# Performance work log

Hardware: AMD Instinct MI355X
Metric: run time of the kernel (lower is better)

Reference implementation:

```python
import jax, jax.numpy as jnp
import numpy as np

D = 1024
LD = 64
NTR = 8192
NT = 8192
DY = 128

def setup_inputs() -> dict:
    key = jax.random.key(0)
    k1, k2, k3, k4 = jax.random.split(key, 4)
    xtr = jax.random.normal(k1, (NTR, D), dtype=jnp.float32)
    ytr = jax.random.normal(k2, (NTR, DY), dtype=jnp.float32)
    xt = jax.random.normal(k3, (NT, D), dtype=jnp.float32)
    A = jax.random.normal(k4, (D, LD), dtype=jnp.float32) / (D ** 0.5)
    return {"xtr": xtr, "ytr": ytr, "xt": xt, "A": A}

def reference(xtr, ytr, xt, A):
    # mean-center both train and test features with the train mean
    mu = jnp.mean(xtr, axis=0, keepdims=True)          # [1, d]
    qtr = (xtr - mu) @ A                                # [Ntr, ld]
    qt = (xt - mu) @ A                                  # [Nt, ld]
    scores = jnp.einsum('nl,ml->nm', qt, qtr)           # [Nt, Ntr]
    E = jax.nn.softmax(scores, axis=1)                  # row-wise softmax over train points
    return E @ ytr                                      # [Nt, dy]
```

## Files before the change

kernel.cpp:

```cpp
#include <hip/hip_runtime.h>
#include <hip/hip_bf16.h>

#define D    1024
#define LD   64
#define NTR  8192
#define NT   8192
#define DY   128

#define SHIFT 40.0f
#define NCHUNK 8
#define CHUNK (NTR / NCHUNK)

typedef __attribute__((ext_vector_type(8))) short bf16x8;
typedef __attribute__((ext_vector_type(4))) short short4_;
typedef __attribute__((ext_vector_type(4))) float f4;

static __device__ __forceinline__ short f2bf(float f) {
    __hip_bfloat16 h = __float2bfloat16(f);
    short s; __builtin_memcpy(&s, &h, 2); return s;
}
static __device__ __forceinline__ float bf2f(short s) {
    __hip_bfloat16 h; __builtin_memcpy(&h, &s, 2); return __bfloat162float(h);
}

static __device__ __forceinline__ void gload_lds16(const void* g, void* l) {
    __builtin_amdgcn_global_load_lds(
        (const __attribute__((address_space(1))) unsigned int*)g,
        (__attribute__((address_space(3))) unsigned int*)l,
        16, 0, 0);
}

__global__ __launch_bounds__(256) void proj_prep(const float* __restrict__ xt,
                                                 const float* __restrict__ xtr,
                                                 const float* __restrict__ A,
                                                 const float* __restrict__ ytr,
                                                 short* __restrict__ qt_hi,
                                                 short* __restrict__ qt_lo,
                                                 short* __restrict__ ktr_hi,
                                                 short* __restrict__ ktr_lo,
                                                 float* __restrict__ muAp,
                                                 short* __restrict__ vtile) {
    __shared__ __align__(16) float smem[4224];

    int tid = threadIdx.x;
    int b = blockIdx.x;

    if (b >= 1024) {
        float* tile = smem;
        int bz = b - 1024;
        int t0 = (bz & 127) * 64;
        int d0 = (bz >> 7) * 64;
        int c = tid & 63;
        int r4 = tid >> 6;
        #pragma unroll
        for (int i = 0; i < 16; ++i) {
            int r = i * 4 + r4;
            tile[r * 66 + c] = ytr[(long)(t0 + r) * DY + d0 + c];
        }
        __syncthreads();
        #pragma unroll
        for (int i = 0; i < 16; ++i) {
            int r = i * 4 + r4;
            int t = t0 + c;
            int dy = d0 + r;
            long idx = (long)(t >> 5) * 4096 + (long)dy * 32
                     + ((((t >> 3) & 3) ^ (dy & 3)) << 3) + (t & 7);
            vtile[idx] = f2bf(tile[c * 66 + r]);
        }
        return;
    }

    float (*xbuf)[2][1024] = (float (*)[2][1024])smem;

    int wave = tid >> 6;
    int lane = tid & 63;
    int quad = lane >> 4;
    int l16 = lane & 15;

    bool is_test = b < (NT / 16);
    int row0 = (is_test ? b : b - NT / 16) * 16;
    const float* x = is_test ? xt : xtr;

    int lr = wave * 4 + (lane >> 4);
    int cg = (lane & 15) ^ (lr & 7);
    const float* xsrc = x + (long)(row0 + lr) * D + cg * 4;

    int col = wave * 16 + l16;
    const float* Acol = A + col;

    f4 acc = (f4){0.f, 0.f, 0.f, 0.f};

    int pr0 = ((quad * 2) ^ (l16 & 7)) * 4;
    int pr1 = (((quad * 2) | 1) ^ (l16 & 7)) * 4;

    gload_lds16(xsrc, &xbuf[0][0][wave * 256]);
    gload_lds16(xsrc + 64, &xbuf[0][1][wave * 256]);
    __syncthreads();

    #pragma unroll 1
    for (int s = 0; s < 8; ++s) {
        int cur = s & 1;
        if (s < 7) {
            const float* nsrc = xsrc + (s + 1) * 128;
            gload_lds16(nsrc, &xbuf[cur ^ 1][0][wave * 256]);
            gload_lds16(nsrc + 64, &xbuf[cur ^ 1][1][wave * 256]);
        }

        #pragma unroll
        for (int s2 = 0; s2 < 2; ++s2) {
            int k0 = s * 128 + s2 * 64;

            bf16x8 bh0, bh1, bl0, bl1;
            #pragma unroll
            for (int j = 0; j < 8; ++j) {
                float a0 = Acol[(long)(k0 + quad * 8 + j) * LD];
                float a1 = Acol[(long)(k0 + 32 + quad * 8 + j) * LD];
                short h0 = f2bf(a0);
                short h1 = f2bf(a1);
                bh0[j] = h0; bl0[j] = f2bf(a0 - bf2f(h0));
                bh1[j] = h1; bl1[j] = f2bf(a1 - bf2f(h1));
            }

            const float* xrow = &xbuf[cur][s2][l16 * 64];
            bf16x8 ah[2], al[2];
            #pragma unroll
            for (int h = 0; h < 2; ++h) {
                f4 v0 = *(const f4*)(xrow + h * 32 + pr0);
                f4 v1 = *(const f4*)(xrow + h * 32 + pr1);
                #pragma unroll
                for (int e = 0; e < 4; ++e) {
                    short hi0 = f2bf(v0[e]);
                    short hi1 = f2bf(v1[e]);
                    ah[h][e]     = hi0;
                    ah[h][e + 4] = hi1;
                    al[h][e]     = f2bf(v0[e] - bf2f(hi0));
                    al[h][e + 4] = f2bf(v1[e] - bf2f(hi1));
                }
            }
            acc = __builtin_amdgcn_mfma_f32_16x16x32_bf16(ah[0], bh0, acc, 0, 0, 0);
            acc = __builtin_amdgcn_mfma_f32_16x16x32_bf16(al[0], bh0, acc, 0, 0, 0);
            acc = __builtin_amdgcn_mfma_f32_16x16x32_bf16(ah[0], bl0, acc, 0, 0, 0);
            acc = __builtin_amdgcn_mfma_f32_16x16x32_bf16(ah[1], bh1, acc, 0, 0, 0);
            acc = __builtin_amdgcn_mfma_f32_16x16x32_bf16(al[1], bh1, acc, 0, 0, 0);
            acc = __builtin_amdgcn_mfma_f32_16x16x32_bf16(ah[1], bl1, acc, 0, 0, 0);
        }
        __syncthreads();
    }

    #pragma unroll
    for (int r = 0; r < 4; ++r) {
        int grow = row0 + quad * 4 + r;
        float qv = acc[r];
        short hi = f2bf(qv);
        short lo = f2bf(qv - bf2f(hi));
        if (is_test) {
            qt_hi[(long)grow * LD + col] = hi;
            qt_lo[(long)grow * LD + col] = lo;
        } else {
            int tl = grow & 31;
            long idx = (long)(grow >> 5) * 2048 + tl * 64
                     + ((((col >> 3) ^ (tl & 7))) << 3) + (col & 7);
            ktr_hi[idx] = hi;
            ktr_lo[idx] = lo;
        }
    }

    if (!is_test) {
        float s = acc[0] + acc[1] + acc[2] + acc[3];
        s += __shfl_xor(s, 16);
        s += __shfl_xor(s, 32);
        if (quad == 0) muAp[(long)(b - NT / 16) * 64 + col] = s;
    }
}

__global__ __launch_bounds__(256) void c_kernel(const short* __restrict__ ktr_hi,
                                                const short* __restrict__ ktr_lo,
                                                const float* __restrict__ muAp,
                                                float* __restrict__ cc) {
    __shared__ float red[4][64];
    __shared__ __align__(16) float muAs[64];
    int l = threadIdx.x & 63;
    int g = threadIdx.x >> 6;
    float ms = 0.f;
    #pragma unroll 8
    for (int p = g; p < 512; p += 4) ms += muAp[(long)p * 64 + l];
    red[g][l] = ms;
    __syncthreads();
    if (threadIdx.x < 64)
        muAs[l] = (red[0][l] + red[1][l] + red[2][l] + red[3][l]) *
                  (1.0f / (float)NTR);
    __syncthreads();

    int t = blockIdx.x * 256 + threadIdx.x;
    int tl = t & 31;
    long rb = (long)(t >> 5) * 2048 + tl * 64;
    float s = SHIFT;
    #pragma unroll
    for (int c = 0; c < 8; ++c) {
        int pos = (c ^ (tl & 7)) << 3;
        bf16x8 h8 = *(const bf16x8*)&ktr_hi[rb + pos];
        bf16x8 l8 = *(const bf16x8*)&ktr_lo[rb + pos];
        f4 m0 = *(const f4*)&muAs[c * 8];
        f4 m1 = *(const f4*)&muAs[c * 8 + 4];
        #pragma unroll
        for (int j = 0; j < 4; ++j) {
            s += (bf2f(h8[j]) + bf2f(l8[j])) * m0[j];
            s += (bf2f(h8[j + 4]) + bf2f(l8[j + 4])) * m1[j];
        }
    }
    cc[t] = s;
}

__global__ __launch_bounds__(256, 2) void flash_kernel(const short* __restrict__ qt_hi,
                                                       const short* __restrict__ qt_lo,
                                                       const short* __restrict__ ksw_hi,
                                                       const short* __restrict__ ksw_lo,
                                                       const short* __restrict__ vtile,
                                                       const float* __restrict__ cc,
                                                       float* __restrict__ Opart,
                                                       float* __restrict__ Lpart) {
    __shared__ __align__(16) short kbh[2][2048];
    __shared__ __align__(16) short kbl[2][2048];
    __shared__ __align__(16) short vbuf[2][4096];
    __shared__ __align__(16) short ptile[4][1280];

    int tid = threadIdx.x;
    int wave = tid >> 6;
    int lane = tid & 63;
    int quad = lane >> 4;
    int l16 = lane & 15;

    int kc = blockIdx.x & 7;
    int qi = blockIdx.x >> 3;
    int q0w = qi * 128 + wave * 32;
    int tile0 = kc * 32;
    int kc0 = kc * CHUNK;

    int soff = wave * 512 + lane * 8;
    int ldso = wave * 512;

    bf16x8 qh[2][2], ql[2][2];
    #pragma unroll
    for (int rt = 0; rt < 2; ++rt) {
        const short* qrh = qt_hi + (long)(q0w + rt * 16 + l16) * LD + quad * 8;
        const short* qrl = qt_lo + (long)(q0w + rt * 16 + l16) * LD + quad * 8;
        qh[rt][0] = *(const bf16x8*)qrh;
        qh[rt][1] = *(const bf16x8*)(qrh + 32);
        ql[rt][0] = *(const bf16x8*)qrl;
        ql[rt][1] = *(const bf16x8*)(qrl + 32);
    }

    bf16x8 onef;
    #pragma unroll
    for (int i = 0; i < 8; ++i) onef[i] = (short)0x3F80;

    f4 Ov[2][8];
    f4 Lv[2];
    #pragma unroll
    for (int rt = 0; rt < 2; ++rt) {
        Lv[rt] = (f4){0.f, 0.f, 0.f, 0.f};
        #pragma unroll
        for (int jt = 0; jt < 8; ++jt) Ov[rt][jt] = (f4){0.f, 0.f, 0.f, 0.f};
    }

    short* myp = &ptile[wave][0];
    const int p0 = ((quad ^ (l16 & 7)) << 3);
    const int pv = ((quad ^ (l16 & 3)) << 3);

    gload_lds16(ksw_hi + (long)tile0 * 2048 + soff, &kbh[0][ldso]);
    gload_lds16(ksw_lo + (long)tile0 * 2048 + soff, &kbl[0][ldso]);
    gload_lds16(vtile + (long)tile0 * 4096 + soff, &vbuf[0][ldso]);
    gload_lds16(vtile + (long)tile0 * 4096 + 2048 + soff, &vbuf[0][2048 + ldso]);
    __syncthreads();

    #pragma unroll 1
    for (int it = 0; it < 32; ++it) {
        int cur = it & 1;

        f4 cv[2];
        #pragma unroll
        for (int tt = 0; tt < 2; ++tt)
            cv[tt] = *(const f4*)&cc[kc0 + it * 32 + tt * 16 + quad * 4];

        if (it < 31) {
            int nb = cur ^ 1;
            long tb = (long)(tile0 + it + 1);
            gload_lds16(ksw_hi + tb * 2048 + soff, &kbh[nb][ldso]);
            gload_lds16(ksw_lo + tb * 2048 + soff, &kbl[nb][ldso]);
            gload_lds16(vtile + tb * 4096 + soff, &vbuf[nb][ldso]);
            gload_lds16(vtile + tb * 4096 + 2048 + soff, &vbuf[nb][2048 + ldso]);
        }

        bf16x8 kh[2][2], kl[2][2];
        #pragma unroll
        for (int tt = 0; tt < 2; ++tt) {
            int rb = (tt * 16 + l16) * 64;
            kh[tt][0] = *(const bf16x8*)&kbh[cur][rb + p0];
            kh[tt][1] = *(const bf16x8*)&kbh[cur][rb + (p0 ^ 32)];
            kl[tt][0] = *(const bf16x8*)&kbl[cur][rb + p0];
            kl[tt][1] = *(const bf16x8*)&kbl[cur][rb + (p0 ^ 32)];
        }

        f4 s[2][2];
        #pragma unroll
        for (int rt = 0; rt < 2; ++rt) {
            #pragma unroll
            for (int tt = 0; tt < 2; ++tt) {
                f4 a = (f4){0.f, 0.f, 0.f, 0.f};
                a = __builtin_amdgcn_mfma_f32_16x16x32_bf16(kh[tt][0], qh[rt][0], a, 0, 0, 0);
                a = __builtin_amdgcn_mfma_f32_16x16x32_bf16(kh[tt][0], ql[rt][0], a, 0, 0, 0);
                a = __builtin_amdgcn_mfma_f32_16x16x32_bf16(kh[tt][1], qh[rt][1], a, 0, 0, 0);
                a = __builtin_amdgcn_mfma_f32_16x16x32_bf16(kh[tt][1], ql[rt][1], a, 0, 0, 0);
                a = __builtin_amdgcn_mfma_f32_16x16x32_bf16(kl[tt][0], qh[rt][0], a, 0, 0, 0);
                a = __builtin_amdgcn_mfma_f32_16x16x32_bf16(kl[tt][1], qh[rt][1], a, 0, 0, 0);
                s[rt][tt] = a;
            }
        }

        #pragma unroll
        for (int rt = 0; rt < 2; ++rt) {
            #pragma unroll
            for (int tt = 0; tt < 2; ++tt) {
                short4_ p4;
                p4[0] = f2bf(__expf(s[rt][tt][0] - cv[tt][0]));
                p4[1] = f2bf(__expf(s[rt][tt][1] - cv[tt][1]));
                p4[2] = f2bf(__expf(s[rt][tt][2] - cv[tt][2]));
                p4[3] = f2bf(__expf(s[rt][tt][3] - cv[tt][3]));
                *(short4_*)&myp[(rt * 16 + l16) * 40 + tt * 16 + quad * 4] = p4;
            }
        }

        bf16x8 vf[8];
        #pragma unroll
        for (int jt = 0; jt < 8; ++jt)
            vf[jt] = *(const bf16x8*)&vbuf[cur][(jt * 16 + l16) * 32 + pv];
        #pragma unroll
        for (int rt = 0; rt < 2; ++rt) {
            bf16x8 pf = *(const bf16x8*)&myp[(rt * 16 + l16) * 40 + quad * 8];
            #pragma unroll
            for (int jt = 0; jt < 8; ++jt)
                Ov[rt][jt] = __builtin_amdgcn_mfma_f32_16x16x32_bf16(pf, vf[jt], Ov[rt][jt], 0, 0, 0);
            Lv[rt] = __builtin_amdgcn_mfma_f32_16x16x32_bf16(pf, onef, Lv[rt], 0, 0, 0);
        }

        __syncthreads();
    }

    long ob = (long)kc * NT;
    #pragma unroll
    for (int rt = 0; rt < 2; ++rt) {
        #pragma unroll
        for (int jt = 0; jt < 8; ++jt) {
            #pragma unroll
            for (int r = 0; r < 4; ++r)
                Opart[(ob + q0w + rt * 16 + quad * 4 + r) * DY + jt * 16 + l16] =
                    Ov[rt][jt][r];
        }
        if (l16 == 0) {
            #pragma unroll
            for (int r = 0; r < 4; ++r)
                Lpart[ob + q0w + rt * 16 + quad * 4 + r] = Lv[rt][r];
        }
    }
}

__global__ __launch_bounds__(256) void finalize_kernel(const float* __restrict__ Opart,
                                                       const float* __restrict__ Lpart,
                                                       float* __restrict__ out) {
    long i = ((long)blockIdx.x * 256 + threadIdx.x) * 8;
    long row = i >> 7;
    float L = 0.f;
    f4 a = (f4){0.f, 0.f, 0.f, 0.f};
    f4 b = (f4){0.f, 0.f, 0.f, 0.f};
    #pragma unroll
    for (int kc = 0; kc < NCHUNK; ++kc) {
        L += Lpart[(long)kc * NT + row];
        const float* p = &Opart[((long)kc * NT) * DY + i];
        a += *(const f4*)p;
        b += *(const f4*)(p + 4);
    }
    float linv = 1.0f / L;
    a *= linv; b *= linv;
    *(f4*)&out[i] = a;
    *(f4*)&out[i + 4] = b;
}

extern "C" void kernel_launch(void* const* d_in, const int* in_sizes, int n_in,
                              void* d_out, int out_size, void* d_ws, size_t ws_size,
                              hipStream_t stream) {
    const float* xtr = (const float*)d_in[0];
    const float* ytr = (const float*)d_in[1];
    const float* xt  = (const float*)d_in[2];
    const float* A   = (const float*)d_in[3];
    float* out = (float*)d_out;

    char* w = (char*)d_ws;
    float* muAp  = (float*)w; w += (size_t)512 * 64 * 4;
    float* cc    = (float*)w; w += (size_t)NTR * 4;
    float* Lpart = (float*)w; w += (size_t)NCHUNK * NT * 4;
    float* Opart = (float*)w; w += (size_t)NCHUNK * NT * DY * 4;
    short* qt_hi  = (short*)w; w += (size_t)NT * LD * 2;
    short* qt_lo  = (short*)w; w += (size_t)NT * LD * 2;
    short* ksw_hi = (short*)w; w += (size_t)NTR * LD * 2;
    short* ksw_lo = (short*)w; w += (size_t)NTR * LD * 2;
    short* vtile  = (short*)w; w += (size_t)DY * NTR * 2;
    (void)ws_size; (void)in_sizes; (void)n_in; (void)out_size;

    proj_prep<<<1280, 256, 0, stream>>>(xt, xtr, A, ytr,
                                        qt_hi, qt_lo, ksw_hi, ksw_lo, muAp, vtile);
    c_kernel<<<32, 256, 0, stream>>>(ksw_hi, ksw_lo, muAp, cc);
    flash_kernel<<<512, 256, 0, stream>>>(qt_hi, qt_lo, ksw_hi, ksw_lo, vtile, cc,
                                          Opart, Lpart);
    finalize_kernel<<<(NT * DY) / (256 * 8), 256, 0, stream>>>(Opart, Lpart, out);
}
```

Before: 177.0 us.

## Switch QK scores to fp16 split-Q, single-fp16 K, and bf16 partial outputs

Replaces the bf16 hi/lo split for both Q and K with fp16, keeping a hi/lo split only for Q and storing K as a single fp16 value. Score MFMAs per tile drop from six to four, and the K low-part buffer and its loads are removed. Partial O outputs are written as bf16 instead of fp32, halving that write and read traffic, and the flash kernel's launch bound is raised to 4 blocks per CU. Dropping the K low part and storing partials in bf16 lowers precision, and fp16 K has a narrower range than bf16.

Measured after the change: 218.4 us. +23.4%, slower.

```diff
diff --git a/kernel.cpp b/kernel.cpp
--- a/kernel.cpp
+++ b/kernel.cpp
@@ -12,6 +12,7 @@
 #define CHUNK (NTR / NCHUNK)
 
 typedef __attribute__((ext_vector_type(8))) short bf16x8;
+typedef __attribute__((ext_vector_type(8))) _Float16 half8;
 typedef __attribute__((ext_vector_type(4))) short short4_;
 typedef __attribute__((ext_vector_type(4))) float f4;
 
@@ -21,6 +22,13 @@
 }
 static __device__ __forceinline__ float bf2f(short s) {
     __hip_bfloat16 h; __builtin_memcpy(&h, &s, 2); return __bfloat162float(h);
+}
+static __device__ __forceinline__ short f2h(float f) {
+    _Float16 h = (_Float16)f;
+    short s; __builtin_memcpy(&s, &h, 2); return s;
+}
+static __device__ __forceinline__ float h2f(short s) {
+    _Float16 h; __builtin_memcpy(&h, &s, 2); return (float)h;
 }
 
 static __device__ __forceinline__ void gload_lds16(const void* g, void* l) {
@@ -36,8 +44,7 @@
                                                  const float* __restrict__ ytr,
                                                  short* __restrict__ qt_hi,
                                                  short* __restrict__ qt_lo,
-                                                 short* __restrict__ ktr_hi,
-                                                 short* __restrict__ ktr_lo,
+                                                 short* __restrict__ ktr,
                                                  float* __restrict__ muAp,
                                                  short* __restrict__ vtile) {
     __shared__ __align__(16) float smem[4224];
@@ -151,17 +158,15 @@
     for (int r = 0; r < 4; ++r) {
         int grow = row0 + quad * 4 + r;
         float qv = acc[r];
-        short hi = f2bf(qv);
-        short lo = f2bf(qv - bf2f(hi));
         if (is_test) {
+            short hi = f2h(qv);
             qt_hi[(long)grow * LD + col] = hi;
-            qt_lo[(long)grow * LD + col] = lo;
+            qt_lo[(long)grow * LD + col] = f2h(qv - h2f(hi));
         } else {
             int tl = grow & 31;
             long idx = (long)(grow >> 5) * 2048 + tl * 64
                      + ((((col >> 3) ^ (tl & 7))) << 3) + (col & 7);
-            ktr_hi[idx] = hi;
-            ktr_lo[idx] = lo;
+            ktr[idx] = f2h(qv);
         }
     }
 
@@ -173,8 +178,7 @@
     }
 }
 
-__global__ __launch_bounds__(256) void c_kernel(const short* __restrict__ ktr_hi,
-                                                const short* __restrict__ ktr_lo,
+__global__ __launch_bounds__(256) void c_kernel(const short* __restrict__ ktr,
                                                 const float* __restrict__ muAp,
                                                 float* __restrict__ cc) {
     __shared__ float red[4][64];
@@ -198,29 +202,26 @@
     #pragma unroll
     for (int c = 0; c < 8; ++c) {
         int pos = (c ^ (tl & 7)) << 3;
-        bf16x8 h8 = *(const bf16x8*)&ktr_hi[rb + pos];
-        bf16x8 l8 = *(const bf16x8*)&ktr_lo[rb + pos];
+        bf16x8 h8 = *(const bf16x8*)&ktr[rb + pos];
         f4 m0 = *(const f4*)&muAs[c * 8];
         f4 m1 = *(const f4*)&muAs[c * 8 + 4];
         #pragma unroll
         for (int j = 0; j < 4; ++j) {
-            s += (bf2f(h8[j]) + bf2f(l8[j])) * m0[j];
-            s += (bf2f(h8[j + 4]) + bf2f(l8[j + 4])) * m1[j];
+            s += h2f(h8[j]) * m0[j];
+            s += h2f(h8[j + 4]) * m1[j];
         }
     }
     cc[t] = s;
 }
 
-__global__ __launch_bounds__(256, 2) void flash_kernel(const short* __restrict__ qt_hi,
+__global__ __launch_bounds__(256, 4) void flash_kernel(const short* __restrict__ qt_hi,
                                                        const short* __restrict__ qt_lo,
-                                                       const short* __restrict__ ksw_hi,
-                                                       const short* __restrict__ ksw_lo,
+                                                       const short* __restrict__ ksw,
                                                        const short* __restrict__ vtile,
                                                        const float* __restrict__ cc,
-                                                       float* __restrict__ Opart,
+                                                       short* __restrict__ Opart,
                                                        float* __restrict__ Lpart) {
     __shared__ __align__(16) short kbh[2][2048];
-    __shared__ __align__(16) short kbl[2][2048];
     __shared__ __align__(16) short vbuf[2][4096];
     __shared__ __align__(16) short ptile[4][1280];
 
@@ -239,15 +240,15 @@
     int soff = wave * 512 + lane * 8;
     int ldso = wave * 512;
 
-    bf16x8 qh[2][2], ql[2][2];
+    half8 qh[2][2], ql[2][2];
     #pragma unroll
     for (int rt = 0; rt < 2; ++rt) {
         const short* qrh = qt_hi + (long)(q0w + rt * 16 + l16) * LD + quad * 8;
         const short* qrl = qt_lo + (long)(q0w + rt * 16 + l16) * LD + quad * 8;
-        qh[rt][0] = *(const bf16x8*)qrh;
-        qh[rt][1] = *(const bf16x8*)(qrh + 32);
-        ql[rt][0] = *(const bf16x8*)qrl;
-        ql[rt][1] = *(const bf16x8*)(qrl + 32);
+        qh[rt][0] = *(const half8*)qrh;
+        qh[rt][1] = *(const half8*)(qrh + 32);
+        ql[rt][0] = *(const half8*)qrl;
+        ql[rt][1] = *(const half8*)(qrl + 32);
     }
 
     bf16x8 onef;
@@ -267,8 +268,7 @@
     const int p0 = ((quad ^ (l16 & 7)) << 3);
     const int pv = ((quad ^ (l16 & 3)) << 3);
 
-    gload_lds16(ksw_hi + (long)tile0 * 2048 + soff, &kbh[0][ldso]);
-    gload_lds16(ksw_lo + (long)tile0 * 2048 + soff, &kbl[0][ldso]);
+    gload_lds16(ksw + (long)tile0 * 2048 + soff, &kbh[0][ldso]);
     gload_lds16(vtile + (long)tile0 * 4096 + soff, &vbuf[0][ldso]);
     gload_lds16(vtile + (long)tile0 * 4096 + 2048 + soff, &vbuf[0][2048 + ldso]);
     __syncthreads();
@@ -285,20 +285,17 @@
         if (it < 31) {
             int nb = cur ^ 1;
             long tb = (long)(tile0 + it + 1);
-            gload_lds16(ksw_hi + tb * 2048 + soff, &kbh[nb][ldso]);
-            gload_lds16(ksw_lo + tb * 2048 + soff, &kbl[nb][ldso]);
+            gload_lds16(ksw + tb * 2048 + soff, &kbh[nb][ldso]);
             gload_lds16(vtile + tb * 4096 + soff, &vbuf[nb][ldso]);
             gload_lds16(vtile + tb * 4096 + 2048 + soff, &vbuf[nb][2048 + ldso]);
         }
 
-        bf16x8 kh[2][2], kl[2][2];
+        half8 kh[2][2];
         #pragma unroll
         for (int tt = 0; tt < 2; ++tt) {
             int rb = (tt * 16 + l16) * 64;
-            kh[tt][0] = *(const bf16x8*)&kbh[cur][rb + p0];
-            kh[tt][1] = *(const bf16x8*)&kbh[cur][rb + (p0 ^ 32)];
-            kl[tt][0] = *(const bf16x8*)&kbl[cur][rb + p0];
-            kl[tt][1] = *(const bf16x8*)&kbl[cur][rb + (p0 ^ 32)];
+            kh[tt][0] = *(const half8*)&kbh[cur][rb + p0];
+            kh[tt][1] = *(const half8*)&kbh[cur][rb + (p0 ^ 32)];
         }
 
         f4 s[2][2];
@@ -307,12 +304,10 @@
             #pragma unroll
             for (int tt = 0; tt < 2; ++tt) {
                 f4 a = (f4){0.f, 0.f, 0.f, 0.f};
-                a = __builtin_amdgcn_mfma_f32_16x16x32_bf16(kh[tt][0], qh[rt][0], a, 0, 0, 0);
-                a = __builtin_amdgcn_mfma_f32_16x16x32_bf16(kh[tt][0], ql[rt][0], a, 0, 0, 0);
-                a = __builtin_amdgcn_mfma_f32_16x16x32_bf16(kh[tt][1], qh[rt][1], a, 0, 0, 0);
-                a = __builtin_amdgcn_mfma_f32_16x16x32_bf16(kh[tt][1], ql[rt][1], a, 0, 0, 0);
-                a = __builtin_amdgcn_mfma_f32_16x16x32_bf16(kl[tt][0], qh[rt][0], a, 0, 0, 0);
-                a = __builtin_amdgcn_mfma_f32_16x16x32_bf16(kl[tt][1], qh[rt][1], a, 0, 0, 0);
+                a = __builtin_amdgcn_mfma_f32_16x16x32_f16(kh[tt][0], qh[rt][0], a, 0, 0, 0);
+                a = __builtin_amdgcn_mfma_f32_16x16x32_f16(kh[tt][0], ql[rt][0], a, 0, 0, 0);
+                a = __builtin_amdgcn_mfma_f32_16x16x32_f16(kh[tt][1], qh[rt][1], a, 0, 0, 0);
+                a = __builtin_amdgcn_mfma_f32_16x16x32_f16(kh[tt][1], ql[rt][1], a, 0, 0, 0);
                 s[rt][tt] = a;
             }
         }
@@ -354,7 +349,7 @@
             #pragma unroll
             for (int r = 0; r < 4; ++r)
                 Opart[(ob + q0w + rt * 16 + quad * 4 + r) * DY + jt * 16 + l16] =
-                    Ov[rt][jt][r];
+                    f2bf(Ov[rt][jt][r]);
         }
         if (l16 == 0) {
             #pragma unroll
@@ -364,7 +359,7 @@
     }
 }
 
-__global__ __launch_bounds__(256) void finalize_kernel(const float* __restrict__ Opart,
+__global__ __launch_bounds__(256) void finalize_kernel(const short* __restrict__ Opart,
                                                        const float* __restrict__ Lpart,
                                                        float* __restrict__ out) {
     long i = ((long)blockIdx.x * 256 + threadIdx.x) * 8;
@@ -375,9 +370,12 @@
     #pragma unroll
     for (int kc = 0; kc < NCHUNK; ++kc) {
         L += Lpart[(long)kc * NT + row];
-        const float* p = &Opart[((long)kc * NT) * DY + i];
-        a += *(const f4*)p;
-        b += *(const f4*)(p + 4);
+        bf16x8 o = *(const bf16x8*)&Opart[(long)kc * NT * DY + i];
+        #pragma unroll
+        for (int j = 0; j < 4; ++j) {
+            a[j] += bf2f(o[j]);
+            b[j] += bf2f(o[j + 4]);
+        }
     }
     float linv = 1.0f / L;
     a *= linv; b *= linv;
@@ -398,18 +396,17 @@
     float* muAp  = (float*)w; w += (size_t)512 * 64 * 4;
     float* cc    = (float*)w; w += (size_t)NTR * 4;
     float* Lpart = (float*)w; w += (size_t)NCHUNK * NT * 4;
-    float* Opart = (float*)w; w += (size_t)NCHUNK * NT * DY * 4;
+    short* Opart = (short*)w; w += (size_t)NCHUNK * NT * DY * 2;
     short* qt_hi  = (short*)w; w += (size_t)NT * LD * 2;
     short* qt_lo  = (short*)w; w += (size_t)NT * LD * 2;
-    short* ksw_hi = (short*)w; w += (size_t)NTR * LD * 2;
-    short* ksw_lo = (short*)w; w += (size_t)NTR * LD * 2;
+    short* ksw    = (short*)w; w += (size_t)NTR * LD * 2;
     short* vtile  = (short*)w; w += (size_t)DY * NTR * 2;
     (void)ws_size; (void)in_sizes; (void)n_in; (void)out_size;
 
     proj_prep<<<1280, 256, 0, stream>>>(xt, xtr, A, ytr,
-                                        qt_hi, qt_lo, ksw_hi, ksw_lo, muAp, vtile);
-    c_kernel<<<32, 256, 0, stream>>>(ksw_hi, ksw_lo, muAp, cc);
-    flash_kernel<<<512, 256, 0, stream>>>(qt_hi, qt_lo, ksw_hi, ksw_lo, vtile, cc,
+                                        qt_hi, qt_lo, ksw, muAp, vtile);
+    c_kernel<<<32, 256, 0, stream>>>(ksw, muAp, cc);
+    flash_kernel<<<512, 256, 0, stream>>>(qt_hi, qt_lo, ksw, vtile, cc,
                                           Opart, Lpart);
     finalize_kernel<<<(NT * DY) / (256 * 8), 256, 0, stream>>>(Opart, Lpart, out);
 }
```
